# Kernel optimization log

Measured on AMD Instinct MI355X. Metric: run time of the kernel, lower is better.

Reference implementation:

```python
import jax, jax.numpy as jnp
import numpy as np

N = 100000
NEG_SLOPE = 0.2
EPS = 1e-16


def _leaky_relu(x):
    return jnp.where(x > 0, x, NEG_SLOPE * x)


def gat_conv(x, src, dst, W, a_src, a_dst, b, heads, out_ch):
    # x: [N, F_in], W: [F_in, heads*out_ch], a_src/a_dst: [heads, out_ch], b: [heads*out_ch]
    h = (x @ W).reshape(N, heads, out_ch)                     # [N, H, C]
    alpha_s = jnp.einsum('nhc,hc->nh', h, a_src)              # [N, H]
    alpha_d = jnp.einsum('nhc,hc->nh', h, a_dst)              # [N, H]
    e = _leaky_relu(alpha_s[src] + alpha_d[dst])              # [E, H]
    # softmax over incoming edges per destination node
    m = jax.ops.segment_max(e, dst, num_segments=N)           # [N, H]
    ee = jnp.exp(e - m[dst])
    denom = jax.ops.segment_sum(ee, dst, num_segments=N)      # [N, H]
    alpha = ee / (denom[dst] + EPS)                           # [E, H]
    msg = h[src] * alpha[:, :, None]                          # [E, H, C]
    out = jax.ops.segment_sum(msg, dst, num_segments=N)       # [N, H, C]
    return out.reshape(N, heads * out_ch) + b


def setup_inputs() -> dict:
    key = jax.random.key(0)
    ks = jax.random.split(key, 16)
    x = jax.random.normal(ks[0], (N, 128), dtype=jnp.float32)
    edge_index = jax.random.randint(ks[1], (2, 1600000), 0, N, dtype=jnp.int64)
    s = 0.1
    return {
        'x': x,
        'edge_index': edge_index,
        'W0': jax.random.normal(ks[2], (128, 4 * 32), dtype=jnp.float32) * s,
        'asrc0': jax.random.normal(ks[3], (4, 32), dtype=jnp.float32) * s,
        'adst0': jax.random.normal(ks[4], (4, 32), dtype=jnp.float32) * s,
        'b0': jnp.zeros((128,), dtype=jnp.float32),
        'W1': jax.random.normal(ks[5], (128, 4 * 32), dtype=jnp.float32) * s,
        'asrc1': jax.random.normal(ks[6], (4, 32), dtype=jnp.float32) * s,
        'adst1': jax.random.normal(ks[7], (4, 32), dtype=jnp.float32) * s,
        'b1': jnp.zeros((128,), dtype=jnp.float32),
        'W2': jax.random.normal(ks[8], (128, 1 * 32), dtype=jnp.float32) * s,
        'asrc2': jax.random.normal(ks[9], (1, 32), dtype=jnp.float32) * s,
        'adst2': jax.random.normal(ks[10], (1, 32), dtype=jnp.float32) * s,
        'b2': jnp.zeros((32,), dtype=jnp.float32),
    }


def reference(x, edge_index, W0, asrc0, adst0, b0, W1, asrc1, adst1, b1, W2, asrc2, adst2, b2):
    # PyG GATConv default add_self_loops=True
    loops = jnp.arange(N, dtype=edge_index.dtype)
    src = jnp.concatenate([edge_index[0], loops])
    dst = jnp.concatenate([edge_index[1], loops])
    # dropout layers are identity in eval mode
    h = gat_conv(x, src, dst, W0, asrc0, adst0, b0, heads=4, out_ch=32)
    h = jax.nn.relu(h)
    h = gat_conv(h, src, dst, W1, asrc1, adst1, b1, heads=4, out_ch=32)
    h = jax.nn.relu(h)
    out = gat_conv(h, src, dst, W2, asrc2, adst2, b2, heads=1, out_ch=32)
    return out
```

## Files before the change

### kernel.cpp

```cpp
#include <hip/hip_runtime.h>
#include <hip/hip_fp16.h>

#define NEG_SLOPE 0.2f
#define EPSV 1e-16f
#define NXCD 8
#define BCAP2 448
#define EPB 8192

typedef _Float16 half8 __attribute__((ext_vector_type(8)));
typedef float floatx4 __attribute__((ext_vector_type(4)));

__device__ __forceinline__ float leaky_relu(float v) {
    return v > 0.f ? v : NEG_SLOPE * v;
}

__global__ __launch_bounds__(256)
void wconv3_kernel(const float* __restrict__ W0, const float* __restrict__ W1,
                   const float* __restrict__ W2, __half* __restrict__ Wt0,
                   __half* __restrict__ Wt1, __half* __restrict__ Wt2,
                   int* __restrict__ bcur, int nbx)
{
    const int idx = blockIdx.x * 256 + threadIdx.x;
    if (idx < nbx) bcur[idx] = 0;
    if (idx < 16384) {
        const int k = idx >> 7, c = idx & 127;
        Wt0[c * 128 + k] = __float2half(W0[idx]);
    } else if (idx < 32768) {
        const int i = idx - 16384;
        const int k = i >> 7, c = i & 127;
        Wt1[c * 128 + k] = __float2half(W1[i]);
    } else if (idx < 36864) {
        const int i = idx - 32768;
        const int k = i >> 5, c = i & 31;
        Wt2[c * 128 + k] = __float2half(W2[i]);
    }
}

template<int HC, typename XT>
__global__ __launch_bounds__(256)
void mfma_gemm_kernel(const XT* __restrict__ X, const __half* __restrict__ Wt,
                      const float* __restrict__ asrc, const float* __restrict__ adst,
                      __half* __restrict__ Hout, float* __restrict__ as_,
                      float* __restrict__ ad_, int nrows)
{
    constexpr int NH = HC / 32;
    const int wid = (blockIdx.x * 256 + threadIdx.x) >> 6;
    const int lane = threadIdx.x & 63;
    const int row0 = wid * 16;
    if (row0 >= nrows) return;
    const int r = lane & 15;
    const int kq = lane >> 4;
    const int arow = min(row0 + r, nrows - 1);

    half8 a[4];
    #pragma unroll
    for (int kk = 0; kk < 4; ++kk) {
        const int k0 = kk * 32 + kq * 8;
        if constexpr (sizeof(XT) == 4) {
            const float4 f0 = *(const float4*)&X[(size_t)arow * 128 + k0];
            const float4 f1 = *(const float4*)&X[(size_t)arow * 128 + k0 + 4];
            half8 v;
            v[0] = (_Float16)f0.x; v[1] = (_Float16)f0.y;
            v[2] = (_Float16)f0.z; v[3] = (_Float16)f0.w;
            v[4] = (_Float16)f1.x; v[5] = (_Float16)f1.y;
            v[6] = (_Float16)f1.z; v[7] = (_Float16)f1.w;
            a[kk] = v;
        } else {
            a[kk] = *(const half8*)&X[(size_t)arow * 128 + k0];
        }
    }

    float asp[NH][4];
    float adp[NH][4];
    #pragma unroll
    for (int hh = 0; hh < NH; ++hh)
        #pragma unroll
        for (int j = 0; j < 4; ++j) { asp[hh][j] = 0.f; adp[hh][j] = 0.f; }

    #pragma unroll
    for (int ct = 0; ct < HC / 16; ++ct) {
        floatx4 acc = {0.f, 0.f, 0.f, 0.f};
        #pragma unroll
        for (int kk = 0; kk < 4; ++kk) {
            const half8 b = *(const half8*)&Wt[(size_t)(ct * 16 + r) * 128 + kk * 32 + kq * 8];
            acc = __builtin_amdgcn_mfma_f32_16x16x32_f16(a[kk], b, acc, 0, 0, 0);
        }
        const float avs = asrc[ct * 16 + r];
        const float avd = adst[ct * 16 + r];
        #pragma unroll
        for (int j = 0; j < 4; ++j) {
            asp[ct / 2][j] = fmaf(acc[j], avs, asp[ct / 2][j]);
            adp[ct / 2][j] = fmaf(acc[j], avd, adp[ct / 2][j]);
        }
        #pragma unroll
        for (int j = 0; j < 4; ++j) {
            const int orow = row0 + kq * 4 + j;
            if (orow < nrows)
                Hout[(size_t)orow * HC + ct * 16 + r] = __float2half(acc[j]);
        }
    }

    #pragma unroll
    for (int off = 1; off < 16; off <<= 1) {
        #pragma unroll
        for (int hh = 0; hh < NH; ++hh)
            #pragma unroll
            for (int j = 0; j < 4; ++j) {
                asp[hh][j] += __shfl_xor(asp[hh][j], off);
                adp[hh][j] += __shfl_xor(adp[hh][j], off);
            }
    }
    if constexpr (NH == 4) {
        #pragma unroll
        for (int j = 0; j < 4; ++j) {
            const int row = row0 + kq * 4 + j;
            if (row < nrows) {
                #pragma unroll
                for (int hh = 0; hh < 4; ++hh) {
                    if (r == j * 4 + hh) {
                        as_[row * 4 + hh] = asp[hh][j];
                        ad_[row * 4 + hh] = adp[hh][j];
                    }
                }
            }
        }
    } else {
        #pragma unroll
        for (int j = 0; j < 4; ++j) {
            const int row = row0 + kq * 4 + j;
            if (row < nrows) {
                if (r == j)     as_[row] = asp[0][j];
                if (r == j + 8) ad_[row] = adp[0][j];
            }
        }
    }
}

__global__ __launch_bounds__(256)
void bucket_append_kernel(const int* __restrict__ srcs, const int* __restrict__ dsts,
                          int E, int NB, int* __restrict__ bcur,
                          unsigned* __restrict__ packed)
{
    __shared__ int hist[1024];
    __shared__ int cursor[1024];
    const int t = threadIdx.x;
    const int xcd = blockIdx.x & (NXCD - 1);
    const int base = blockIdx.x * EPB;

    for (int i = t; i < NB; i += 256) hist[i] = 0;
    __syncthreads();
    for (int k = 0; k < EPB / 256; ++k) {
        const int e = base + k * 256 + t;
        if (e < E) atomicAdd(&hist[dsts[e] >> 7], 1);
    }
    __syncthreads();
    for (int i = t; i < NB; i += 256) {
        const int c = hist[i];
        cursor[i] = (c > 0) ? atomicAdd(&bcur[i * NXCD + xcd], c) : 0;
    }
    __syncthreads();
    for (int k = 0; k < EPB / 256; ++k) {
        const int e = base + k * 256 + t;
        if (e < E) {
            const int s = srcs[e];
            const int d = dsts[e];
            const int b = d >> 7;
            const int p = atomicAdd(&cursor[b], 1);
            if (p < BCAP2)
                packed[(size_t)(b * NXCD + xcd) * BCAP2 + p] =
                    (unsigned)s | ((unsigned)(d & 127) << 20);
        }
    }
}

__global__ __launch_bounds__(256)
void scanB_kernel(const int* __restrict__ bcur, int* __restrict__ bbase,
                  int* __restrict__ row_ptr, int NB, int N)
{
    __shared__ int lds[256];
    const int t = threadIdx.x;
    int v0 = 0, v1 = 0, v2 = 0, v3 = 0;
    #pragma unroll
    for (int j = 0; j < 4; ++j) {
        const int i = t * 4 + j;
        int s = 0;
        if (i < NB) {
            s = min(128, N - i * 128);
            #pragma unroll
            for (int x = 0; x < NXCD; ++x)
                s += min(bcur[i * NXCD + x], BCAP2);
        }
        if (j == 0) v0 = s; else if (j == 1) v1 = s; else if (j == 2) v2 = s; else v3 = s;
    }
    const int tsum = v0 + v1 + v2 + v3;
    lds[t] = tsum;
    __syncthreads();
    for (int off = 1; off < 256; off <<= 1) {
        const int y = (t >= off) ? lds[t - off] : 0;
        __syncthreads();
        lds[t] += y;
        __syncthreads();
    }
    int excl = lds[t] - tsum;
    if (t * 4 + 0 < NB) bbase[t * 4 + 0] = excl; excl += v0;
    if (t * 4 + 1 < NB) bbase[t * 4 + 1] = excl; excl += v1;
    if (t * 4 + 2 < NB) bbase[t * 4 + 2] = excl; excl += v2;
    if (t * 4 + 3 < NB) bbase[t * 4 + 3] = excl;
    if (t == 255) row_ptr[N] = lds[255];
}

__global__ __launch_bounds__(256)
void bucket_scatter_kernel(const unsigned* __restrict__ packed, const int* __restrict__ bcur,
                           const int* __restrict__ bbase, int* __restrict__ row_ptr,
                           int* __restrict__ col, int N)
{
    __shared__ int cnt[128];
    __shared__ int cur[128];
    const int t = threadIdx.x;
    const int b = blockIdx.x;
    const int nbase = b * 128;
    const int nvalid = min(128, N - nbase);
    if (t < 128) cnt[t] = (t < nvalid) ? 1 : 0;
    __syncthreads();
    #pragma unroll
    for (int x = 0; x < NXCD; ++x) {
        const int sb = b * NXCD + x;
        const int n = min(bcur[sb], BCAP2);
        const unsigned* bp = packed + (size_t)sb * BCAP2;
        for (int i = t; i < n; i += 256)
            atomicAdd(&cnt[bp[i] >> 20], 1);
    }
    __syncthreads();
    int myc = 0;
    if (t < 128) { myc = cnt[t]; cur[t] = myc; }
    __syncthreads();
    for (int off = 1; off < 128; off <<= 1) {
        int y = 0;
        if (t < 128 && t >= off) y = cur[t - off];
        __syncthreads();
        if (t < 128) cur[t] += y;
        __syncthreads();
    }
    if (t < 128) {
        const int base = bbase[b] + cur[t] - myc;
        if (t < nvalid) row_ptr[nbase + t] = base;
        cur[t] = base;
    }
    __syncthreads();
    if (t < nvalid) {
        const int p = atomicAdd(&cur[t], 1);
        col[p] = nbase + t;
    }
    #pragma unroll
    for (int x = 0; x < NXCD; ++x) {
        const int sb = b * NXCD + x;
        const int n = min(bcur[sb], BCAP2);
        const unsigned* bp = packed + (size_t)sb * BCAP2;
        for (int i = t; i < n; i += 256) {
            const unsigned en = bp[i];
            const int p = atomicAdd(&cur[en >> 20], 1);
            col[p] = en & 0xFFFFF;
        }
    }
}

template<int H>
__global__ __launch_bounds__(256)
void gather_kernel(const int* __restrict__ row_ptr, const int* __restrict__ col,
                   const float* __restrict__ as_, const float* __restrict__ ad_,
                   const __half* __restrict__ hbuf, const float* __restrict__ bias,
                   __half* __restrict__ hin, float* __restrict__ outf, int N)
{
    __shared__ float pS[4][64 * H];
    __shared__ int   sS[4][64];
    const int w = threadIdx.x >> 6;
    const int lane = threadIdx.x & 63;
    const int d = blockIdx.x * 4 + w;
    if (d >= N) return;
    const int jb = __builtin_amdgcn_readfirstlane(row_ptr[d]);
    const int je = __builtin_amdgcn_readfirstlane(row_ptr[d + 1]);

    float ad0 = 0.f, ad1 = 0.f, ad2 = 0.f, ad3 = 0.f;
    if (H == 4) {
        const float4 adv = *(const float4*)&ad_[d * 4];
        ad0 = adv.x; ad1 = adv.y; ad2 = adv.z; ad3 = adv.w;
    } else {
        ad0 = ad_[d];
    }

    float s0 = 0.f, s1 = 0.f, s2 = 0.f, s3 = 0.f;
    float a0 = 0.f, a1 = 0.f, a2 = 0.f, a3 = 0.f;
    float a4 = 0.f, a5 = 0.f, a6 = 0.f, a7 = 0.f;
    const int q4 = lane >> 4;
    const int cq = lane & 15;
    const int h4 = cq >> 2;
    const int q16 = lane >> 2;
    const int c16 = (lane & 3) * 8;

    for (int cb = jb; cb < je; cb += 64) {
        const int j = cb + lane;
        const int cnt = min(64, je - cb);
        int sreg = 0;
        float p0 = 0.f, p1 = 0.f, p2 = 0.f, p3 = 0.f;
        if (j < je) {
            sreg = col[j];
            if (H == 4) {
                const float4 a = *(const float4*)&as_[sreg * 4];
                p0 = __expf(leaky_relu(a.x + ad0)); s0 += p0;
                p1 = __expf(leaky_relu(a.y + ad1)); s1 += p1;
                p2 = __expf(leaky_relu(a.z + ad2)); s2 += p2;
                p3 = __expf(leaky_relu(a.w + ad3)); s3 += p3;
            } else {
                p0 = __expf(leaky_relu(as_[sreg] + ad0)); s0 += p0;
            }
        }
        __builtin_amdgcn_wave_barrier();
        sS[w][lane] = sreg;
        if (H == 4) {
            *(float4*)&pS[w][lane * 4] = make_float4(p0, p1, p2, p3);
        } else {
            pS[w][lane] = p0;
        }
        __builtin_amdgcn_wave_barrier();
        if (H == 4) {
            #pragma unroll 4
            for (int e2 = q4; e2 < cnt; e2 += 4) {
                const int s2v = sS[w][e2];
                const float pp = pS[w][e2 * 4 + h4];
                const half8 v = *(const half8*)&hbuf[(size_t)s2v * 128 + cq * 8];
                a0 = fmaf(pp, (float)v[0], a0);
                a1 = fmaf(pp, (float)v[1], a1);
                a2 = fmaf(pp, (float)v[2], a2);
                a3 = fmaf(pp, (float)v[3], a3);
                a4 = fmaf(pp, (float)v[4], a4);
                a5 = fmaf(pp, (float)v[5], a5);
                a6 = fmaf(pp, (float)v[6], a6);
                a7 = fmaf(pp, (float)v[7], a7);
            }
        } else {
            #pragma unroll 4
            for (int e2 = q16; e2 < cnt; e2 += 16) {
                const int s2v = sS[w][e2];
                const float pp = pS[w][e2];
                const half8 v = *(const half8*)&hbuf[(size_t)s2v * 32 + c16];
                a0 = fmaf(pp, (float)v[0], a0);
                a1 = fmaf(pp, (float)v[1], a1);
                a2 = fmaf(pp, (float)v[2], a2);
                a3 = fmaf(pp, (float)v[3], a3);
                a4 = fmaf(pp, (float)v[4], a4);
                a5 = fmaf(pp, (float)v[5], a5);
                a6 = fmaf(pp, (float)v[6], a6);
                a7 = fmaf(pp, (float)v[7], a7);
            }
        }
        __builtin_amdgcn_wave_barrier();
    }

    #pragma unroll
    for (int off = 32; off >= 1; off >>= 1) {
        s0 += __shfl_xor(s0, off);
        if (H == 4) {
            s1 += __shfl_xor(s1, off);
            s2 += __shfl_xor(s2, off);
            s3 += __shfl_xor(s3, off);
        }
    }
    if (H == 4) {
        a0 += __shfl_xor(a0, 16); a0 += __shfl_xor(a0, 32);
        a1 += __shfl_xor(a1, 16); a1 += __shfl_xor(a1, 32);
        a2 += __shfl_xor(a2, 16); a2 += __shfl_xor(a2, 32);
        a3 += __shfl_xor(a3, 16); a3 += __shfl_xor(a3, 32);
        a4 += __shfl_xor(a4, 16); a4 += __shfl_xor(a4, 32);
        a5 += __shfl_xor(a5, 16); a5 += __shfl_xor(a5, 32);
        a6 += __shfl_xor(a6, 16); a6 += __shfl_xor(a6, 32);
        a7 += __shfl_xor(a7, 16); a7 += __shfl_xor(a7, 32);
        if (lane < 16) {
            const float sh = (h4 == 0) ? s0 : (h4 == 1) ? s1 : (h4 == 2) ? s2 : s3;
            const float inv = 1.f / (sh + EPSV);
            const int c0 = cq * 8;
            const float4 b0v = *(const float4*)&bias[c0];
            const float4 b1v = *(const float4*)&bias[c0 + 4];
            union { __half2 h2[4]; float4 f4; } u;
            u.h2[0] = __floats2half2_rn(fmaxf(fmaf(a0, inv, b0v.x), 0.f),
                                        fmaxf(fmaf(a1, inv, b0v.y), 0.f));
            u.h2[1] = __floats2half2_rn(fmaxf(fmaf(a2, inv, b0v.z), 0.f),
                                        fmaxf(fmaf(a3, inv, b0v.w), 0.f));
            u.h2[2] = __floats2half2_rn(fmaxf(fmaf(a4, inv, b1v.x), 0.f),
                                        fmaxf(fmaf(a5, inv, b1v.y), 0.f));
            u.h2[3] = __floats2half2_rn(fmaxf(fmaf(a6, inv, b1v.z), 0.f),
                                        fmaxf(fmaf(a7, inv, b1v.w), 0.f));
            *(float4*)&hin[(size_t)d * 128 + c0] = u.f4;
        }
    } else {
        a0 += __shfl_xor(a0, 4); a0 += __shfl_xor(a0, 8); a0 += __shfl_xor(a0, 16); a0 += __shfl_xor(a0, 32);
        a1 += __shfl_xor(a1, 4); a1 += __shfl_xor(a1, 8); a1 += __shfl_xor(a1, 16); a1 += __shfl_xor(a1, 32);
        a2 += __shfl_xor(a2, 4); a2 += __shfl_xor(a2, 8); a2 += __shfl_xor(a2, 16); a2 += __shfl_xor(a2, 32);
        a3 += __shfl_xor(a3, 4); a3 += __shfl_xor(a3, 8); a3 += __shfl_xor(a3, 16); a3 += __shfl_xor(a3, 32);
        a4 += __shfl_xor(a4, 4); a4 += __shfl_xor(a4, 8); a4 += __shfl_xor(a4, 16); a4 += __shfl_xor(a4, 32);
        a5 += __shfl_xor(a5, 4); a5 += __shfl_xor(a5, 8); a5 += __shfl_xor(a5, 16); a5 += __shfl_xor(a5, 32);
        a6 += __shfl_xor(a6, 4); a6 += __shfl_xor(a6, 8); a6 += __shfl_xor(a6, 16); a6 += __shfl_xor(a6, 32);
        a7 += __shfl_xor(a7, 4); a7 += __shfl_xor(a7, 8); a7 += __shfl_xor(a7, 16); a7 += __shfl_xor(a7, 32);
        if (lane < 4) {
            const float inv = 1.f / (s0 + EPSV);
            const float4 bb0 = *(const float4*)&bias[c16];
            const float4 bb1 = *(const float4*)&bias[c16 + 4];
            *(float4*)&outf[(size_t)d * 32 + c16] =
                make_float4(fmaf(a0, inv, bb0.x), fmaf(a1, inv, bb0.y),
                            fmaf(a2, inv, bb0.z), fmaf(a3, inv, bb0.w));
            *(float4*)&outf[(size_t)d * 32 + c16 + 4] =
                make_float4(fmaf(a4, inv, bb1.x), fmaf(a5, inv, bb1.y),
                            fmaf(a6, inv, bb1.z), fmaf(a7, inv, bb1.w));
        }
    }
}

extern "C" void kernel_launch(void* const* d_in, const int* in_sizes, int n_in,
                              void* d_out, int out_size, void* d_ws, size_t ws_size,
                              hipStream_t stream)
{
    const float* x     = (const float*)d_in[0];
    const int*   ei    = (const int*)d_in[1];
    const float* W0    = (const float*)d_in[2];
    const float* asrc0 = (const float*)d_in[3];
    const float* adst0 = (const float*)d_in[4];
    const float* b0    = (const float*)d_in[5];
    const float* W1    = (const float*)d_in[6];
    const float* asrc1 = (const float*)d_in[7];
    const float* adst1 = (const float*)d_in[8];
    const float* b1    = (const float*)d_in[9];
    const float* W2    = (const float*)d_in[10];
    const float* asrc2 = (const float*)d_in[11];
    const float* adst2 = (const float*)d_in[12];
    const float* b2    = (const float*)d_in[13];

    const int N = in_sizes[0] / 128;
    const int E = in_sizes[1] / 2;
    const int Etot = E + N;
    const int NB = (N + 127) / 128;
    const int* srcs = ei;
    const int* dsts = ei + E;

    __half* hbuf    = (__half*)d_ws;
    __half* hin     = hbuf + (size_t)N * 128;
    float* as_      = (float*)(hin + (size_t)N * 128);
    float* ad_      = as_ + (size_t)N * 4;
    __half* Wt0     = (__half*)(ad_ + (size_t)N * 4);
    __half* Wt1     = Wt0 + 128 * 128;
    __half* Wt2     = Wt1 + 128 * 128;
    int* row_ptr    = (int*)(Wt2 + 32 * 128);
    int* bbase      = row_ptr + N + 1;
    int* col        = bbase + NB;
    int* bcur       = col + Etot;
    unsigned* packed = (unsigned*)(bcur + NB * NXCD);

    const dim3 blk(256);
    const int gemm_grid    = ((N + 15) / 16 + 3) / 4;
    const int append_grid  = (E + EPB - 1) / EPB;
    const int gather_grid  = (N + 3) / 4;

    wconv3_kernel<<<(36864 + 255) / 256, blk, 0, stream>>>(W0, W1, W2, Wt0, Wt1, Wt2,
                                                           bcur, NB * NXCD);
    bucket_append_kernel<<<append_grid, blk, 0, stream>>>(srcs, dsts, E, NB, bcur, packed);
    scanB_kernel<<<1, blk, 0, stream>>>(bcur, bbase, row_ptr, NB, N);
    bucket_scatter_kernel<<<NB, blk, 0, stream>>>(packed, bcur, bbase, row_ptr, col, N);

    mfma_gemm_kernel<128, float><<<gemm_grid, blk, 0, stream>>>(
        x, Wt0, asrc0, adst0, hbuf, as_, ad_, N);
    gather_kernel<4><<<gather_grid, blk, 0, stream>>>(row_ptr, col, as_, ad_, hbuf, b0, hin, nullptr, N);

    mfma_gemm_kernel<128, __half><<<gemm_grid, blk, 0, stream>>>(
        hin, Wt1, asrc1, adst1, hbuf, as_, ad_, N);
    gather_kernel<4><<<gather_grid, blk, 0, stream>>>(row_ptr, col, as_, ad_, hbuf, b1, hin, nullptr, N);

    mfma_gemm_kernel<32, __half><<<gemm_grid, blk, 0, stream>>>(
        hin, Wt2, asrc2, adst2, hbuf, as_, ad_, N);
    gather_kernel<1><<<gather_grid, blk, 0, stream>>>(row_ptr, col, as_, ad_, hbuf, b2, nullptr, (float*)d_out, N);
}
```

Before: 363.5 us.

## Fuse edge bucket append with layer-0 GEMM in one heterogeneous launch

Merges the CSR bucket-append kernel and the first-layer MFMA GEMM into a single launch whose blocks split by index: the first blocks do edge bucketing, the rest compute x@W0 and the attention logits. The two pieces of work are independent, so running them concurrently lets the memory-bound append overlap the GEMM and removes one kernel launch. The fused kernel's register and LDS footprint is the maximum of both paths, which may lower occupancy for the GEMM blocks, and the GEMM now runs before the scan/scatter rather than after.

Result: faster. 343.7 us (-5.5%).

```diff
diff --git a/kernel.cpp b/kernel.cpp
--- a/kernel.cpp
+++ b/kernel.cpp
@@ -37,15 +37,13 @@
 }
 
 template<int HC, typename XT>
-__global__ __launch_bounds__(256)
-void mfma_gemm_kernel(const XT* __restrict__ X, const __half* __restrict__ Wt,
-                      const float* __restrict__ asrc, const float* __restrict__ adst,
-                      __half* __restrict__ Hout, float* __restrict__ as_,
-                      float* __restrict__ ad_, int nrows)
+__device__ __forceinline__
+void gemm_body(int wid, int lane, const XT* __restrict__ X, const __half* __restrict__ Wt,
+               const float* __restrict__ asrc, const float* __restrict__ adst,
+               __half* __restrict__ Hout, float* __restrict__ as_,
+               float* __restrict__ ad_, int nrows)
 {
     constexpr int NH = HC / 32;
-    const int wid = (blockIdx.x * 256 + threadIdx.x) >> 6;
-    const int lane = threadIdx.x & 63;
     const int row0 = wid * 16;
     if (row0 >= nrows) return;
     const int r = lane & 15;
@@ -136,16 +134,24 @@
     }
 }
 
+template<int HC, typename XT>
 __global__ __launch_bounds__(256)
-void bucket_append_kernel(const int* __restrict__ srcs, const int* __restrict__ dsts,
-                          int E, int NB, int* __restrict__ bcur,
-                          unsigned* __restrict__ packed)
-{
-    __shared__ int hist[1024];
-    __shared__ int cursor[1024];
-    const int t = threadIdx.x;
-    const int xcd = blockIdx.x & (NXCD - 1);
-    const int base = blockIdx.x * EPB;
+void mfma_gemm_kernel(const XT* __restrict__ X, const __half* __restrict__ Wt,
+                      const float* __restrict__ asrc, const float* __restrict__ adst,
+                      __half* __restrict__ Hout, float* __restrict__ as_,
+                      float* __restrict__ ad_, int nrows)
+{
+    const int wid = (blockIdx.x * 256 + threadIdx.x) >> 6;
+    gemm_body<HC, XT>(wid, threadIdx.x & 63, X, Wt, asrc, adst, Hout, as_, ad_, nrows);
+}
+
+__device__ __forceinline__
+void append_body(int bid, int t, const int* __restrict__ srcs, const int* __restrict__ dsts,
+                 int E, int NB, int* __restrict__ bcur, unsigned* __restrict__ packed,
+                 int* hist, int* cursor)
+{
+    const int xcd = bid & (NXCD - 1);
+    const int base = bid * EPB;
 
     for (int i = t; i < NB; i += 256) hist[i] = 0;
     __syncthreads();
@@ -170,6 +176,25 @@
                 packed[(size_t)(b * NXCD + xcd) * BCAP2 + p] =
                     (unsigned)s | ((unsigned)(d & 127) << 20);
         }
+    }
+}
+
+__global__ __launch_bounds__(256)
+void fused_csr_gemm0_kernel(const int* __restrict__ srcs, const int* __restrict__ dsts,
+                            int E, int NB, int* __restrict__ bcur,
+                            unsigned* __restrict__ packed,
+                            const float* __restrict__ x, const __half* __restrict__ Wt0,
+                            const float* __restrict__ asrc0, const float* __restrict__ adst0,
+                            __half* __restrict__ hbuf, float* __restrict__ as_,
+                            float* __restrict__ ad_, int N, int nAppend)
+{
+    __shared__ int hist[1024];
+    __shared__ int cursor[1024];
+    if (blockIdx.x < (unsigned)nAppend) {
+        append_body(blockIdx.x, threadIdx.x, srcs, dsts, E, NB, bcur, packed, hist, cursor);
+    } else {
+        const int wid = ((blockIdx.x - nAppend) * 256 + threadIdx.x) >> 6;
+        gemm_body<128, float>(wid, threadIdx.x & 63, x, Wt0, asrc0, adst0, hbuf, as_, ad_, N);
     }
 }
 
@@ -460,12 +485,12 @@
 
     wconv3_kernel<<<(36864 + 255) / 256, blk, 0, stream>>>(W0, W1, W2, Wt0, Wt1, Wt2,
                                                            bcur, NB * NXCD);
-    bucket_append_kernel<<<append_grid, blk, 0, stream>>>(srcs, dsts, E, NB, bcur, packed);
+    fused_csr_gemm0_kernel<<<append_grid + gemm_grid, blk, 0, stream>>>(
+        srcs, dsts, E, NB, bcur, packed,
+        x, Wt0, asrc0, adst0, hbuf, as_, ad_, N, append_grid);
     scanB_kernel<<<1, blk, 0, stream>>>(bcur, bbase, row_ptr, NB, N);
     bucket_scatter_kernel<<<NB, blk, 0, stream>>>(packed, bcur, bbase, row_ptr, col, N);
 
-    mfma_gemm_kernel<128, float><<<gemm_grid, blk, 0, stream>>>(
-        x, Wt0, asrc0, adst0, hbuf, as_, ad_, N);
     gather_kernel<4><<<gather_grid, blk, 0, stream>>>(row_ptr, col, as_, ad_, hbuf, b0, hin, nullptr, N);
 
     mfma_gemm_kernel<128, __half><<<gemm_grid, blk, 0, stream>>>(
```
